# Optimization experiments

Hardware: AMD Instinct MI355X
Metric: run time of the kernel (lower is better)

Reference implementation:

```python
import jax, jax.numpy as jnp
import numpy as np

THRESHOLD = 0.3

def setup_inputs() -> dict:
    key = jax.random.key(0)
    ks = jax.random.split(key, 8)
    B, T, N, d = 4, 32, 1024, 2
    hd, od, hs, osz = 64, 64, 128, 2
    p = lambda k, sh: jax.random.normal(k, sh, jnp.float32) * 0.1
    return {
        "points": jax.random.uniform(ks[0], (B, T, N, d), jnp.float32),
        "W1": p(ks[1], (hd, d)),   "b1": jnp.zeros((hd,), jnp.float32),
        "W2": p(ks[2], (od, hd)),  "b2": jnp.zeros((od,), jnp.float32),
        "Wg": p(ks[3], (hd, od)),  "bg": jnp.zeros((hd,), jnp.float32),
        "Wih": p(ks[4], (3 * hs, hd)), "Whh": p(ks[5], (3 * hs, hs)),
        "bih": jnp.zeros((3 * hs,), jnp.float32), "bhh": jnp.zeros((3 * hs,), jnp.float32),
        "Wf": p(ks[6], (osz, hs)), "bf": jnp.zeros((osz,), jnp.float32),
    }

def _gcn_step(pts, W1, b1, W2, b2, Wg, bg):
    # pts: [N, d]. Torch detaches node features & adjacency (no grad to points).
    pts = jax.lax.stop_gradient(pts)
    dist = jnp.linalg.norm(pts[:, None, :] - pts[None, :, :], axis=2)  # [N,N]
    A = (dist < THRESHOLD).astype(pts.dtype)
    dinv = 1.0 / jnp.sqrt(A.sum(axis=1))          # rowsum >= 1 (self-loop)
    An = A * dinv[:, None] * dinv[None, :]        # D^{-1/2} A D^{-1/2}
    x = jax.nn.relu((An @ pts) @ W1.T + b1)       # [N, hd]
    x = jax.nn.relu((An @ x) @ W2.T + b2)         # [N, od]
    return x.mean(axis=0) @ Wg.T + bg             # [hd]

def reference(points, W1, b1, W2, b2, Wg, bg, Wih, Whh, bih, bhh, Wf, bf):
    # GCN per (batch, time): [B, T, hd]
    gcn = jax.vmap(jax.vmap(lambda p: _gcn_step(p, W1, b1, W2, b2, Wg, bg)))(points)
    H = Whh.shape[1]

    def gru_step(h, x):  # torch GRU gate order: r, z, n
        gi = x @ Wih.T + bih
        gh = h @ Whh.T + bhh
        ir, iz, inn = jnp.split(gi, 3)
        hr, hz, hn = jnp.split(gh, 3)
        r = jax.nn.sigmoid(ir + hr)
        z = jax.nn.sigmoid(iz + hz)
        n = jnp.tanh(inn + r * hn)
        h_new = (1.0 - z) * n + z * h
        return h_new, h_new

    h0 = jnp.zeros((H,), points.dtype)
    run = lambda xs: jax.lax.scan(gru_step, h0, xs)[1]   # [T, H]
    hs = jax.vmap(run)(gcn)                              # [B, T, H]
    y = hs @ Wf.T + bf                                   # [B, T, out]
    # torch: per-element gru_out.mean(dim=1, keepdim=True) on [1,T,out] -> [1,1,out], stacked -> [B,1,1,out]
    return y.mean(axis=1, keepdims=True)[:, :, None, :]
```

## Files before the change

kernel.cpp:

```cpp
#include <hip/hip_runtime.h>
#include <hip/hip_bf16.h>
#include <math.h>

#define N_PTS 1024
#define BT    128
typedef unsigned int u32;
typedef __attribute__((ext_vector_type(8))) short short8_t;
typedef __attribute__((ext_vector_type(4))) float f32x4;

__device__ __forceinline__ float bfi(u32 bits16) {
    union { u32 u; float f; } v; v.u = bits16 << 16; return v.f;
}
__device__ __forceinline__ unsigned short f2bf(float f) {
    union { float f; u32 u; } v; v.f = f;
    return (unsigned short)((v.u + 0x7FFFu + ((v.u >> 16) & 1u)) >> 16);
}
__device__ __forceinline__ u32 pkbf(float a, float b) {
    union { __hip_bfloat162 b2; u32 u; } cv;
    cv.b2 = __float22bfloat162_rn(make_float2(a, b));
    return cv.u;
}
__device__ __forceinline__ float ldf(const void* p, int i, bool bf) {
    return bf ? bfi(((const unsigned short*)p)[i]) : ((const float*)p)[i];
}
__device__ __forceinline__ float2 ldp(const void* pbase, int j, bool bf) {
    if (bf) {
        u32 w = ((const u32*)pbase)[j];
        return make_float2(bfi(w & 0xFFFFu), bfi(w >> 16));
    }
    return ((const float2*)pbase)[j];
}
__device__ __forceinline__ bool detect_bf16(const void* pts, int tid, int* s_flag) {
    if (tid < 64) {
        u32 w = ((const u32*)pts)[tid];
        float v = bfi(w & 0xFFFFu);
        bool ok = (v >= 0.0f) && (v <= 1.0f);
        unsigned long long m = __ballot(ok);
        if (tid == 0) *s_flag = (m == 0xFFFFFFFFFFFFFFFFull) ? 1 : 0;
    }
    __syncthreads();
    return *s_flag != 0;
}
__device__ __forceinline__ bool is_nb(float px, float py, float qx, float qy) {
    float dx = px - qx, dy = py - qy;
    float d2 = __fadd_rn(__fmul_rn(dx, dx), __fmul_rn(dy, dy));
    return d2 < 0.09f;
}
__device__ __forceinline__ const void* pts_base(const void* pts, int bt, bool bf) {
    return bf ? (const void*)((const unsigned short*)pts + (size_t)bt * N_PTS * 2)
              : (const void*)((const float*)pts + (size_t)bt * N_PTS * 2);
}
__device__ __forceinline__ void gload16(const u32* g, u32* l) {
    __builtin_amdgcn_global_load_lds((const __attribute__((address_space(1))) u32*)g,
                                     (__attribute__((address_space(3))) u32*)l, 16, 0, 0);
}
__device__ __forceinline__ float rdlane(float v, int i) {
    return __int_as_float(__builtin_amdgcn_readlane(__float_as_int(v), i));
}
__device__ __forceinline__ float sigm(float x) {
    return __fdividef(1.0f, 1.0f + __expf(-x));
}
__device__ __forceinline__ float tanh_f(float x) {
    return fmaf(2.0f, __fdividef(1.0f, 1.0f + __expf(-2.0f * x)), -1.0f);
}

__global__ __launch_bounds__(256) void k1_bm(const void* __restrict__ pts,
                                             float* __restrict__ dinv,
                                             float* __restrict__ gsum,
                                             u32* __restrict__ bm) {
    int blk = blockIdx.x, tid = threadIdx.x;
    int bt = blk >> 2, q = blk & 3;
    __shared__ float2 sp[N_PTS];
    __shared__ int s_flag;
    bool bf = detect_bf16(pts, tid, &s_flag);
    const void* pb = pts_base(pts, bt, bf);
    for (int j = tid; j < N_PTS; j += 256) sp[j] = ldp(pb, j, bf);
    if (blk < 32) gsum[blk * 256 + tid] = 0.0f;
    __syncthreads();
    int i = q * 256 + tid;
    float px = sp[i].x, py = sp[i].y;
    const float4* sp4 = (const float4*)sp;
    u32* bmrow = bm + (size_t)bt * 32768 + i;
    int cnt = 0;
    for (int c = 0; c < 32; c++) {
        u32 m = 0;
#pragma unroll
        for (int h = 0; h < 8; h++) {
            float4 s01 = sp4[c * 16 + 2 * h], s23 = sp4[c * 16 + 2 * h + 1];
            if (is_nb(px, py, s01.x, s01.y)) m |= 1u << (4 * h);
            if (is_nb(px, py, s01.z, s01.w)) m |= 1u << (4 * h + 1);
            if (is_nb(px, py, s23.x, s23.y)) m |= 1u << (4 * h + 2);
            if (is_nb(px, py, s23.z, s23.w)) m |= 1u << (4 * h + 3);
        }
        bmrow[c * 1024] = m;
        cnt += __popc(m);
    }
    dinv[bt * N_PTS + i] = 1.0f / sqrtf((float)cnt);
}

__global__ __launch_bounds__(256) void k3a_x1v(const void* __restrict__ pts,
                                               const void* __restrict__ W1,
                                               const void* __restrict__ b1,
                                               const float* __restrict__ dinv,
                                               const u32* __restrict__ bm,
                                               u32* __restrict__ x1vB) {
    __shared__ u32 pool[10944];
    __shared__ int s_flag;
    float* poolf = (float*)pool;
    float2* sud = (float2*)pool;
    u32* bmL = pool + 2048;
    float* sdiL = poolf + 10496;
    float* b1L = poolf + 10752;
    float* W1L = poolf + 10816;
    int tid = threadIdx.x, lane = tid & 63, w = tid >> 6;
    int l15 = lane & 15, quad = lane >> 4;
    int blk = blockIdx.x, bt = blk & 127, rowblk = blk >> 7;
    int rowbase = rowblk * 256;
    bool bf = detect_bf16(pts, tid, &s_flag);
    const void* pb = pts_base(pts, bt, bf);
    for (int j = tid; j < N_PTS; j += 256) {
        float2 p = ldp(pb, j, bf);
        float d = dinv[bt * N_PTS + j];
        sud[j] = make_float2(d * p.x, d * p.y);
    }
    sdiL[tid] = dinv[bt * N_PTS + rowbase + tid];
    for (int idx = tid; idx < 8192; idx += 256) {
        int c = idx >> 8, r = idx & 255;
        bmL[r * 33 + c] = bm[(size_t)bt * 32768 + c * 1024 + rowbase + r];
    }
    if (tid < 128) W1L[tid] = ldf(W1, tid, bf);
    if (tid < 64)  b1L[tid] = ldf(b1, tid, bf);
    __syncthreads();

    float w0v[4], w1v[4], b1v[4];
#pragma unroll
    for (int nb = 0; nb < 4; nb++) {
        int ch = nb * 16 + l15;
        w0v[nb] = W1L[2 * ch]; w1v[nb] = W1L[2 * ch + 1]; b1v[nb] = b1L[ch];
    }
    f32x4 acc[4][4];
#pragma unroll
    for (int rf = 0; rf < 4; rf++)
#pragma unroll
        for (int nb = 0; nb < 4; nb++)
#pragma unroll
            for (int r = 0; r < 4; r++) acc[rf][nb][r] = 0.0f;

    for (int ks = 0; ks < 32; ks++) {
        const float4* u4 = (const float4*)(sud + ks * 32 + quad * 8);
        float4 U0 = u4[0], U1 = u4[1], U2 = u4[2], U3 = u4[3];
        float pxd[8] = {U0.x, U0.z, U1.x, U1.z, U2.x, U2.z, U3.x, U3.z};
        float pyd[8] = {U0.y, U0.w, U1.y, U1.w, U2.y, U2.w, U3.y, U3.w};
        short8_t bz[4];
#pragma unroll
        for (int nb = 0; nb < 4; nb++) {
            union { short8_t v; u32 d[4]; } cv;
#pragma unroll
            for (int p = 0; p < 4; p++) {
                float z0 = fmaf(pxd[2 * p],     w0v[nb], pyd[2 * p]     * w1v[nb]);
                float z1 = fmaf(pxd[2 * p + 1], w0v[nb], pyd[2 * p + 1] * w1v[nb]);
                cv.d[p] = pkbf(z0, z1);
            }
            bz[nb] = cv.v;
        }
#pragma unroll
        for (int rf = 0; rf < 4; rf++) {
            u32 word = bmL[(w * 64 + rf * 16 + l15) * 33 + ks];
            u32 by = (word >> (quad * 8)) & 0xFFu;
            short8_t av;
#pragma unroll
            for (int i2 = 0; i2 < 8; i2++)
                av[i2] = (by & (1u << i2)) ? (short)0x3F80 : (short)0;
#pragma unroll
            for (int nb = 0; nb < 4; nb++)
                acc[rf][nb] = __builtin_amdgcn_mfma_f32_16x16x32_bf16(av, bz[nb], acc[rf][nb], 0, 0, 0);
        }
    }
    __syncthreads();
    u32* dumpX = pool + 2048;
#pragma unroll
    for (int rf = 0; rf < 4; rf++) {
        float4 dv = *(const float4*)(sdiL + w * 64 + rf * 16 + quad * 4);
        float dva[4] = {dv.x, dv.y, dv.z, dv.w};
#pragma unroll
        for (int nb = 0; nb < 4; nb++) {
            int ch = nb * 16 + l15;
            float xo[4];
#pragma unroll
            for (int r = 0; r < 4; r++) {
                float tq = fmaf(dva[r], acc[rf][nb][r], b1v[nb]);
                xo[r] = dva[r] * fmaxf(tq, 0.0f);
            }
            u32 dbase = (u32)(ch * 132 + w * 32 + rf * 8 + quad * 2);
            *(uint2*)(dumpX + dbase) = make_uint2(pkbf(xo[0], xo[1]), pkbf(xo[2], xo[3]));
        }
    }
    __syncthreads();
    int ch = tid >> 2, seg = tid & 3;
    u32* gbase = x1vB + ((size_t)(bt * 16 + rowblk * 4) * 64) * 36;
#pragma unroll
    for (int t4 = 0; t4 < 4; t4++) {
        const uint4* src = (const uint4*)(dumpX + ch * 132 + t4 * 32 + seg * 8);
        uint4 v0 = src[0], v1 = src[1];
        u32* dst = gbase + ((size_t)(t4 * 64 + ch)) * 36 + seg * 8;
        *(uint4*)dst = v0; *(uint4*)(dst + 4) = v1;
    }
}

__global__ __launch_bounds__(256) void k3_mfma(const void* __restrict__ pts,
                                               const void* __restrict__ W2,
                                               const void* __restrict__ b2,
                                               const float* __restrict__ dinv,
                                               const u32* __restrict__ bm,
                                               const u32* __restrict__ x1vB,
                                               float* __restrict__ gsum) {
    __shared__ u32 pool[15424];
    __shared__ int s_flag;
    float* poolf = (float*)pool;
    int tid = threadIdx.x, lane = tid & 63, w = tid >> 6;
    int l15 = lane & 15, quad = lane >> 4;
    int blk = blockIdx.x, bt = blk & 127, rowblk = blk >> 7;
    bool bf = detect_bf16(pts, tid, &s_flag);

    const u32* xg = x1vB + (size_t)bt * 36864;
    for (int it = w; it < 9; it += 4)
        gload16(xg + it * 256 + lane * 4, pool + 8192 + it * 256 + lane * 4);

    const u32* bg_ = bm + (size_t)bt * 32768 + rowblk * 256;
    for (int idx = tid; idx < 8192; idx += 256) {
        int c = idx >> 8, r = idx & 255;
        pool[idx] = bg_[c * 1024 + r];
    }
    unsigned short* W2B = (unsigned short*)(pool + 12800);
    for (int idx = tid; idx < 4096; idx += 256) {
        int o = idx >> 6, c = idx & 63;
        W2B[o * 72 + c] = f2bf(ldf(W2, idx, bf));
    }
    if (tid < 256) poolf[15104 + tid] = dinv[bt * N_PTS + rowblk * 256 + tid];
    if (tid < 64)  poolf[15360 + tid] = ldf(b2, tid, bf);

    f32x4 acc[4][4];
#pragma unroll
    for (int rf = 0; rf < 4; rf++)
#pragma unroll
        for (int nb = 0; nb < 4; nb++)
#pragma unroll
            for (int r = 0; r < 4; r++) acc[rf][nb][r] = 0.0f;

    for (int t = 0; t < 16; t++) {
        __syncthreads();
        if (t + 1 < 16) {
            u32* dst = pool + ((t & 1) ? 8192 : 10496);
            const u32* src = xg + (t + 1) * 2304;
            for (int it = w; it < 9; it += 4)
                gload16(src + it * 256 + lane * 4, dst + it * 256 + lane * 4);
        }
        const unsigned short* xf = (const unsigned short*)(pool + ((t & 1) ? 10496 : 8192));
#pragma unroll
        for (int ks = 0; ks < 2; ks++) {
            short8_t bq[4];
#pragma unroll
            for (int rf = 0; rf < 4; rf++) {
                u32 mw = pool[(2 * t + ks) * 256 + w * 64 + rf * 16 + l15];
                u32 by = (mw >> (quad * 8)) & 0xFFu;
                short8_t v;
#pragma unroll
                for (int i2 = 0; i2 < 8; i2++)
                    v[i2] = (by & (1u << i2)) ? (short)0x3F80 : (short)0;
                bq[rf] = v;
            }
#pragma unroll
            for (int nb = 0; nb < 4; nb++) {
                short8_t af = *(const short8_t*)(xf + (nb * 16 + l15) * 72 + ks * 32 + quad * 8);
#pragma unroll
                for (int rf = 0; rf < 4; rf++)
                    acc[rf][nb] = __builtin_amdgcn_mfma_f32_16x16x32_bf16(af, bq[rf], acc[rf][nb], 0, 0, 0);
            }
        }
    }
    __syncthreads();

    u32* dump = pool;
#pragma unroll
    for (int rf = 0; rf < 4; rf++) {
        int rn = w * 64 + rf * 16 + l15;
        float di = poolf[15104 + rn];
#pragma unroll
        for (int nb = 0; nb < 4; nb++) {
            u32 lo = (u32)f2bf(acc[rf][nb][0] * di) | ((u32)f2bf(acc[rf][nb][1] * di) << 16);
            u32 hi = (u32)f2bf(acc[rf][nb][2] * di) | ((u32)f2bf(acc[rf][nb][3] * di) << 16);
            u32* dst = dump + rn * 36 + nb * 8 + quad * 2;
            dst[0] = lo; dst[1] = hi;
        }
    }
    __syncthreads();
    f32x4 xacc[4][4];
#pragma unroll
    for (int ob = 0; ob < 4; ob++)
#pragma unroll
        for (int rf = 0; rf < 4; rf++)
#pragma unroll
            for (int r = 0; r < 4; r++) xacc[ob][rf][r] = 0.0f;
#pragma unroll
    for (int ks2 = 0; ks2 < 2; ks2++) {
        short8_t b2f[4];
#pragma unroll
        for (int rf = 0; rf < 4; rf++)
            b2f[rf] = *(const short8_t*)((const unsigned short*)dump +
                        (w * 64 + rf * 16 + l15) * 72 + ks2 * 32 + quad * 8);
#pragma unroll
        for (int ob = 0; ob < 4; ob++) {
            short8_t a2 = *(const short8_t*)(W2B + (ob * 16 + l15) * 72 + ks2 * 32 + quad * 8);
#pragma unroll
            for (int rf = 0; rf < 4; rf++)
                xacc[ob][rf] = __builtin_amdgcn_mfma_f32_16x16x32_bf16(a2, b2f[rf], xacc[ob][rf], 0, 0, 0);
        }
    }
#pragma unroll
    for (int ob = 0; ob < 4; ob++) {
#pragma unroll
        for (int r = 0; r < 4; r++) {
            int o = ob * 16 + quad * 4 + r;
            float bb = poolf[15360 + o];
            float s = 0.0f;
#pragma unroll
            for (int rf = 0; rf < 4; rf++) s += fmaxf(xacc[ob][rf][r] + bb, 0.0f);
            s += __shfl_down(s, 8, 16);
            s += __shfl_down(s, 4, 16);
            s += __shfl_down(s, 2, 16);
            s += __shfl_down(s, 1, 16);
            if (l15 == 0) atomicAdd(&gsum[bt * 64 + o], s);
        }
    }
}

__global__ __launch_bounds__(768, 1) void k4_all(const void* __restrict__ pts,
                                                 const void* __restrict__ Wg,
                                                 const void* __restrict__ bg,
                                                 const void* __restrict__ Wih,
                                                 const void* __restrict__ Whh,
                                                 const void* __restrict__ bih,
                                                 const void* __restrict__ bhh,
                                                 const void* __restrict__ Wf,
                                                 const void* __restrict__ bf_,
                                                 const float* __restrict__ gsum,
                                                 float* __restrict__ out) {
    int b = blockIdx.x, tid = threadIdx.x;
    __shared__ float s_gir[4096];
    __shared__ float s_giz[4096];
    __shared__ float s_gin[4096];
    __shared__ float sWgT[64 * 65];
    __shared__ float s_gm[2048];
    __shared__ float s_x[2048];
    __shared__ float s_pt[2 * 6 * 128];
    __shared__ int s_flag;
    bool bf = detect_bf16(pts, tid, &s_flag);
    for (int idx = tid; idx < 4096; idx += 768) {
        int o = idx >> 6, k = idx & 63;
        sWgT[k * 65 + o] = ldf(Wg, idx, bf);
    }
    for (int idx = tid; idx < 2048; idx += 768)
        s_gm[idx] = gsum[(size_t)b * 2048 + idx] * (1.0f / 1024.0f);
    __syncthreads();
    for (int idx = tid; idx < 2048; idx += 768) {
        int t = idx >> 6, c = idx & 63;
        float s0 = ldf(bg, c, bf), s1 = 0.f, s2 = 0.f, s3 = 0.f;
        const float* gm = s_gm + t * 64;
#pragma unroll
        for (int k = 0; k < 64; k += 4) {
            s0 = fmaf(sWgT[k * 65 + c],       gm[k],     s0);
            s1 = fmaf(sWgT[(k + 1) * 65 + c], gm[k + 1], s1);
            s2 = fmaf(sWgT[(k + 2) * 65 + c], gm[k + 2], s2);
            s3 = fmaf(sWgT[(k + 3) * 65 + c], gm[k + 3], s3);
        }
        s_x[idx] = (s0 + s1) + (s2 + s3);
    }
    __syncthreads();
    int hi = (tid >= 384) ? 1 : 0;
    int r = tid - hi * 384;
    int g = r >> 7;
    int cpart = r & 127;
    int lane = tid & 63;
    int wv = tid >> 6;
    float* gdst = (g == 0) ? s_gir : (g == 1) ? s_giz : s_gin;
    {
        float wvr[64];
        if (bf) {
#pragma unroll
            for (int k = 0; k < 64; k++) wvr[k] = bfi(((const unsigned short*)Wih)[r * 64 + k]);
        } else {
            const float4* wr = (const float4*)Wih + r * 16;
#pragma unroll
            for (int qq = 0; qq < 16; qq++) {
                float4 v = wr[qq];
                wvr[4*qq] = v.x; wvr[4*qq+1] = v.y; wvr[4*qq+2] = v.z; wvr[4*qq+3] = v.w;
            }
        }
        float br = ldf(bih, r, bf);
        for (int t = hi; t < 32; t += 2) {
            float xv = s_x[t * 64 + lane];
            float s0 = br, s1 = 0.f, s2 = 0.f, s3 = 0.f;
#pragma unroll
            for (int k = 0; k < 64; k += 4) {
                s0 = fmaf(wvr[k],     rdlane(xv, k),     s0);
                s1 = fmaf(wvr[k + 1], rdlane(xv, k + 1), s1);
                s2 = fmaf(wvr[k + 2], rdlane(xv, k + 2), s2);
                s3 = fmaf(wvr[k + 3], rdlane(xv, k + 3), s3);
            }
            gdst[t * 128 + cpart] = (s0 + s1) + (s2 + s3);
        }
    }
    float wh2[64];
    {
        int koff = hi * 64;
        if (bf) {
#pragma unroll
            for (int k = 0; k < 64; k++)
                wh2[k] = bfi(((const unsigned short*)Whh)[r * 128 + koff + k]);
        } else {
            const float4* wr = (const float4*)Whh + (r * 128 + koff) / 4;
#pragma unroll
            for (int qq = 0; qq < 16; qq++) {
                float4 v = wr[qq];
                wh2[4*qq] = v.x; wh2[4*qq+1] = v.y; wh2[4*qq+2] = v.z; wh2[4*qq+3] = v.w;
            }
        }
    }
    float bhr = hi ? 0.0f : ldf(bhh, r, bf);
    int slot = g * 2 + hi;
    int cg = hi * 64 + lane;
    float h_self = 0.0f, hsum = 0.0f;
    __syncthreads();

    for (int t = 0; t < 32; t++) {
        float s0 = bhr, s1 = 0.f, s2 = 0.f, s3 = 0.f;
#pragma unroll
        for (int k = 0; k < 64; k += 4) {
            s0 = fmaf(wh2[k],     rdlane(h_self, k),     s0);
            s1 = fmaf(wh2[k + 1], rdlane(h_self, k + 1), s1);
            s2 = fmaf(wh2[k + 2], rdlane(h_self, k + 2), s2);
            s3 = fmaf(wh2[k + 3], rdlane(h_self, k + 3), s3);
        }
        float* buf = s_pt + (t & 1) * 768;
        buf[slot * 128 + cpart] = (s0 + s1) + (s2 + s3);
        __syncthreads();
        float gr = s_gir[t * 128 + cg] + buf[0 * 128 + cg] + buf[1 * 128 + cg];
        float gz = s_giz[t * 128 + cg] + buf[2 * 128 + cg] + buf[3 * 128 + cg];
        float hn = buf[4 * 128 + cg] + buf[5 * 128 + cg];
        float rr = sigm(gr);
        float zz = sigm(gz);
        float gn = fmaf(rr, hn, s_gin[t * 128 + cg]);
        float n  = tanh_f(gn);
        float hnew = fmaf(zz, h_self - n, n);
        h_self = hnew; hsum += hnew;
    }
    float* sfin = s_gm;
    if (wv == 0) sfin[lane] = hsum;
    if (wv == 6) sfin[64 + lane] = hsum;
    __syncthreads();
    if (tid < 128) {
        float hm = sfin[tid] * (1.0f / 32.0f);
        sfin[256 + tid] = ldf(Wf, tid, bf) * hm;
        sfin[384 + tid] = ldf(Wf, 128 + tid, bf) * hm;
    }
    __syncthreads();
    if (tid < 2) {
        float s = ldf(bf_, tid, bf);
        for (int k = 0; k < 128; k++) s += sfin[256 + tid * 128 + k];
        out[b * 2 + tid] = s;
    }
}

extern "C" void kernel_launch(void* const* d_in, const int* in_sizes, int n_in,
                              void* d_out, int out_size, void* d_ws, size_t ws_size,
                              hipStream_t stream) {
    const void* pts = d_in[0];
    const void* W1  = d_in[1];
    const void* b1  = d_in[2];
    const void* W2  = d_in[3];
    const void* b2  = d_in[4];
    const void* Wg  = d_in[5];
    const void* bg  = d_in[6];
    const void* Wih = d_in[7];
    const void* Whh = d_in[8];
    const void* bih = d_in[9];
    const void* bhh = d_in[10];
    const void* Wf  = d_in[11];
    const void* bf_ = d_in[12];

    float* dinv = (float*)d_ws;
    float* gsum = dinv + (size_t)BT * N_PTS;
    u32*   bm   = (u32*)(gsum + BT * 64);
    u32*   x1vB = bm + (size_t)BT * 32768;

    k1_bm  <<<512, 256, 0, stream>>>(pts, dinv, gsum, bm);
    k3a_x1v<<<512, 256, 0, stream>>>(pts, W1, b1, dinv, bm, x1vB);
    k3_mfma<<<512, 256, 0, stream>>>(pts, W2, b2, dinv, bm, x1vB, gsum);
    k4_all <<<4, 768, 0, stream>>>(pts, Wg, bg, Wih, Whh, bih, bhh, Wf, bf_,
                                   gsum, (float*)d_out);
}
```

Measured before the change: 241.1 us.

## Use MFMA for GRU input projection and fp16 dot2 for recurrent matvec

Replaces the scalar readlane-based input-gate projection in the GRU kernel with bf16 MFMA tiles, using hi/lo bf16 splitting to keep accuracy close to fp32. The recurrent Whh matvec now keeps weights packed as fp16 pairs and uses fdot2 on a packed-half hidden state, which halves the readlanes per step. The gate update now runs only on the first 128 threads and publishes h through shared memory, adding a second barrier per timestep. This trades fp16 precision in the recurrence and an extra sync for fewer instructions per step; the GRU kernel is probably a small share of total time.

```diff
diff --git a/kernel.cpp b/kernel.cpp
--- a/kernel.cpp
+++ b/kernel.cpp
@@ -7,6 +7,17 @@
 typedef unsigned int u32;
 typedef __attribute__((ext_vector_type(8))) short short8_t;
 typedef __attribute__((ext_vector_type(4))) float f32x4;
+typedef __fp16 fp16x2 __attribute__((ext_vector_type(2)));
+typedef _Float16 f16x2 __attribute__((ext_vector_type(2)));
+
+#if defined(__has_builtin)
+#if __has_builtin(__builtin_amdgcn_fdot2)
+#define HAVE_FDOT2 1
+#endif
+#endif
+#ifndef HAVE_FDOT2
+#define HAVE_FDOT2 0
+#endif
 
 __device__ __forceinline__ float bfi(u32 bits16) {
     union { u32 u; float f; } v; v.u = bits16 << 16; return v.f;
@@ -20,6 +31,25 @@
     cv.b2 = __float22bfloat162_rn(make_float2(a, b));
     return cv.u;
 }
+__device__ __forceinline__ u32 pkh(float a, float b) {
+    union { fp16x2 h; u32 u; } c; c.h = __builtin_amdgcn_cvt_pkrtz(a, b); return c.u;
+}
+__device__ __forceinline__ unsigned short f16b(float v) {
+    union { fp16x2 h; unsigned short s[2]; } c;
+    c.h = __builtin_amdgcn_cvt_pkrtz(v, 0.0f);
+    return c.s[0];
+}
+#if HAVE_FDOT2
+__device__ __forceinline__ float fdot2h(u32 a, u32 b, float c) {
+    union { u32 u; f16x2 h; } A, B; A.u = a; B.u = b;
+    return __builtin_amdgcn_fdot2(A.h, B.h, c, false);
+}
+#else
+__device__ __forceinline__ float fdot2h(u32 a, u32 b, float c) {
+    union { u32 u; _Float16 h[2]; } A, B; A.u = a; B.u = b;
+    return fmaf((float)A.h[0], (float)B.h[0], fmaf((float)A.h[1], (float)B.h[1], c));
+}
+#endif
 __device__ __forceinline__ float ldf(const void* p, int i, bool bf) {
     return bf ? bfi(((const unsigned short*)p)[i]) : ((const float*)p)[i];
 }
@@ -54,8 +84,8 @@
     __builtin_amdgcn_global_load_lds((const __attribute__((address_space(1))) u32*)g,
                                      (__attribute__((address_space(3))) u32*)l, 16, 0, 0);
 }
-__device__ __forceinline__ float rdlane(float v, int i) {
-    return __int_as_float(__builtin_amdgcn_readlane(__float_as_int(v), i));
+__device__ __forceinline__ u32 rdlaneu(u32 v, int i) {
+    return (u32)__builtin_amdgcn_readlane((int)v, i);
 }
 __device__ __forceinline__ float sigm(float x) {
     return __fdividef(1.0f, 1.0f + __expf(-x));
@@ -352,9 +382,15 @@
     __shared__ float sWgT[64 * 65];
     __shared__ float s_gm[2048];
     __shared__ float s_x[2048];
-    __shared__ float s_pt[2 * 6 * 128];
+    __shared__ float s_pt[768];
+    __shared__ unsigned short s_hp[128];
     __shared__ int s_flag;
     bool bf = detect_bf16(pts, tid, &s_flag);
+    int lane = tid & 63, wv = tid >> 6;
+    int l15 = lane & 15, quad = lane >> 4;
+    int hi = (tid >= 384) ? 1 : 0;
+    int r = tid - hi * 384;
+
     for (int idx = tid; idx < 4096; idx += 768) {
         int o = idx >> 6, k = idx & 63;
         sWgT[k * 65 + o] = ldf(Wg, idx, bf);
@@ -375,98 +411,126 @@
         }
         s_x[idx] = (s0 + s1) + (s2 + s3);
     }
-    __syncthreads();
-    int hi = (tid >= 384) ? 1 : 0;
-    int r = tid - hi * 384;
-    int g = r >> 7;
+    u32 whp[32];
+    {
+        int koff = r * 128 + hi * 64;
+        if (bf) {
+            const u32* wp = (const u32*)Whh + koff / 2;
+#pragma unroll
+            for (int m = 0; m < 32; m++) {
+                u32 wq = wp[m];
+                whp[m] = pkh(bfi(wq & 0xFFFFu), bfi(wq >> 16));
+            }
+        } else {
+            const float2* wp = (const float2*)Whh + koff / 2;
+#pragma unroll
+            for (int m = 0; m < 32; m++) {
+                float2 v = wp[m];
+                whp[m] = pkh(v.x, v.y);
+            }
+        }
+    }
+    float bhr = hi ? 0.0f : ldf(bhh, r, bf);
+    __syncthreads();
+
+    {
+        short8_t Ah[2][2], Al[2][2];
+#pragma unroll
+        for (int mt = 0; mt < 2; mt++)
+#pragma unroll
+            for (int ks = 0; ks < 2; ks++) {
+                const float* xs = s_x + (mt * 16 + l15) * 64 + ks * 32 + quad * 8;
+                short8_t ah, al;
+#pragma unroll
+                for (int i = 0; i < 8; i++) {
+                    float v = xs[i];
+                    unsigned short hb = f2bf(v);
+                    ah[i] = (short)hb;
+                    al[i] = (short)f2bf(v - bfi(hb));
+                }
+                Ah[mt][ks] = ah; Al[mt][ks] = al;
+            }
+#pragma unroll
+        for (int ni = 0; ni < 2; ni++) {
+            int nt = wv * 2 + ni;
+            int c = nt * 16 + l15;
+            float bv = ldf(bih, c, bf);
+            short8_t Bh[2], Bl[2];
+#pragma unroll
+            for (int ks = 0; ks < 2; ks++) {
+                int base = c * 64 + ks * 32 + quad * 8;
+                short8_t bh, bl;
+#pragma unroll
+                for (int i = 0; i < 8; i++) {
+                    float v = ldf(Wih, base + i, bf);
+                    unsigned short hb = f2bf(v);
+                    bh[i] = (short)hb;
+                    bl[i] = (short)f2bf(v - bfi(hb));
+                }
+                Bh[ks] = bh; Bl[ks] = bl;
+            }
+            float* gdst = ((nt >> 3) == 0) ? s_gir : (((nt >> 3) == 1) ? s_giz : s_gin);
+            int cpart = (nt & 7) * 16 + l15;
+#pragma unroll
+            for (int mt = 0; mt < 2; mt++) {
+                f32x4 acc; acc[0] = bv; acc[1] = bv; acc[2] = bv; acc[3] = bv;
+#pragma unroll
+                for (int ks = 0; ks < 2; ks++) {
+                    acc = __builtin_amdgcn_mfma_f32_16x16x32_bf16(Ah[mt][ks], Bh[ks], acc, 0, 0, 0);
+                    acc = __builtin_amdgcn_mfma_f32_16x16x32_bf16(Ah[mt][ks], Bl[ks], acc, 0, 0, 0);
+                    acc = __builtin_amdgcn_mfma_f32_16x16x32_bf16(Al[mt][ks], Bh[ks], acc, 0, 0, 0);
+                }
+#pragma unroll
+                for (int rr2 = 0; rr2 < 4; rr2++) {
+                    int t = mt * 16 + quad * 4 + rr2;
+                    gdst[t * 128 + cpart] = acc[rr2];
+                }
+            }
+        }
+    }
+    int slot = (r >> 7) * 2 + hi;
     int cpart = r & 127;
-    int lane = tid & 63;
-    int wv = tid >> 6;
-    float* gdst = (g == 0) ? s_gir : (g == 1) ? s_giz : s_gin;
-    {
-        float wvr[64];
-        if (bf) {
-#pragma unroll
-            for (int k = 0; k < 64; k++) wvr[k] = bfi(((const unsigned short*)Wih)[r * 64 + k]);
-        } else {
-            const float4* wr = (const float4*)Wih + r * 16;
-#pragma unroll
-            for (int qq = 0; qq < 16; qq++) {
-                float4 v = wr[qq];
-                wvr[4*qq] = v.x; wvr[4*qq+1] = v.y; wvr[4*qq+2] = v.z; wvr[4*qq+3] = v.w;
-            }
-        }
-        float br = ldf(bih, r, bf);
-        for (int t = hi; t < 32; t += 2) {
-            float xv = s_x[t * 64 + lane];
-            float s0 = br, s1 = 0.f, s2 = 0.f, s3 = 0.f;
-#pragma unroll
-            for (int k = 0; k < 64; k += 4) {
-                s0 = fmaf(wvr[k],     rdlane(xv, k),     s0);
-                s1 = fmaf(wvr[k + 1], rdlane(xv, k + 1), s1);
-                s2 = fmaf(wvr[k + 2], rdlane(xv, k + 2), s2);
-                s3 = fmaf(wvr[k + 3], rdlane(xv, k + 3), s3);
-            }
-            gdst[t * 128 + cpart] = (s0 + s1) + (s2 + s3);
-        }
-    }
-    float wh2[64];
-    {
-        int koff = hi * 64;
-        if (bf) {
-#pragma unroll
-            for (int k = 0; k < 64; k++)
-                wh2[k] = bfi(((const unsigned short*)Whh)[r * 128 + koff + k]);
-        } else {
-            const float4* wr = (const float4*)Whh + (r * 128 + koff) / 4;
-#pragma unroll
-            for (int qq = 0; qq < 16; qq++) {
-                float4 v = wr[qq];
-                wh2[4*qq] = v.x; wh2[4*qq+1] = v.y; wh2[4*qq+2] = v.z; wh2[4*qq+3] = v.w;
-            }
-        }
-    }
-    float bhr = hi ? 0.0f : ldf(bhh, r, bf);
-    int slot = g * 2 + hi;
-    int cg = hi * 64 + lane;
     float h_self = 0.0f, hsum = 0.0f;
+    u32 hpreg = 0;
     __syncthreads();
 
     for (int t = 0; t < 32; t++) {
         float s0 = bhr, s1 = 0.f, s2 = 0.f, s3 = 0.f;
 #pragma unroll
-        for (int k = 0; k < 64; k += 4) {
-            s0 = fmaf(wh2[k],     rdlane(h_self, k),     s0);
-            s1 = fmaf(wh2[k + 1], rdlane(h_self, k + 1), s1);
-            s2 = fmaf(wh2[k + 2], rdlane(h_self, k + 2), s2);
-            s3 = fmaf(wh2[k + 3], rdlane(h_self, k + 3), s3);
-        }
-        float* buf = s_pt + (t & 1) * 768;
-        buf[slot * 128 + cpart] = (s0 + s1) + (s2 + s3);
+        for (int m = 0; m < 32; m += 4) {
+            s0 = fdot2h(whp[m],     rdlaneu(hpreg, m),     s0);
+            s1 = fdot2h(whp[m + 1], rdlaneu(hpreg, m + 1), s1);
+            s2 = fdot2h(whp[m + 2], rdlaneu(hpreg, m + 2), s2);
+            s3 = fdot2h(whp[m + 3], rdlaneu(hpreg, m + 3), s3);
+        }
+        s_pt[slot * 128 + cpart] = (s0 + s1) + (s2 + s3);
         __syncthreads();
-        float gr = s_gir[t * 128 + cg] + buf[0 * 128 + cg] + buf[1 * 128 + cg];
-        float gz = s_giz[t * 128 + cg] + buf[2 * 128 + cg] + buf[3 * 128 + cg];
-        float hn = buf[4 * 128 + cg] + buf[5 * 128 + cg];
-        float rr = sigm(gr);
-        float zz = sigm(gz);
-        float gn = fmaf(rr, hn, s_gin[t * 128 + cg]);
-        float n  = tanh_f(gn);
-        float hnew = fmaf(zz, h_self - n, n);
-        h_self = hnew; hsum += hnew;
-    }
-    float* sfin = s_gm;
-    if (wv == 0) sfin[lane] = hsum;
-    if (wv == 6) sfin[64 + lane] = hsum;
+        if (tid < 128) {
+            int c = tid;
+            float gr = s_gir[t * 128 + c] + s_pt[c]       + s_pt[128 + c];
+            float gz = s_giz[t * 128 + c] + s_pt[256 + c] + s_pt[384 + c];
+            float hn = s_pt[512 + c] + s_pt[640 + c];
+            float rr = sigm(gr);
+            float zz = sigm(gz);
+            float n  = tanh_f(fmaf(rr, hn, s_gin[t * 128 + c]));
+            float hnew = fmaf(zz, h_self - n, n);
+            h_self = hnew; hsum += hnew;
+            s_hp[c] = f16b(hnew);
+        }
+        __syncthreads();
+        hpreg = ((const u32*)s_hp)[hi * 32 + (lane & 31)];
+    }
+    if (tid < 128) s_gm[tid] = hsum;
     __syncthreads();
     if (tid < 128) {
-        float hm = sfin[tid] * (1.0f / 32.0f);
-        sfin[256 + tid] = ldf(Wf, tid, bf) * hm;
-        sfin[384 + tid] = ldf(Wf, 128 + tid, bf) * hm;
+        float hm = s_gm[tid] * (1.0f / 32.0f);
+        s_gm[256 + tid] = ldf(Wf, tid, bf) * hm;
+        s_gm[384 + tid] = ldf(Wf, 128 + tid, bf) * hm;
     }
     __syncthreads();
     if (tid < 2) {
         float s = ldf(bf_, tid, bf);
-        for (int k = 0; k < 128; k++) s += sfin[256 + tid * 128 + k];
+        for (int k = 0; k < 128; k++) s += s_gm[256 + tid * 128 + k];
         out[b * 2 + tid] = s;
     }
 }
```

Result: no change. 240.8 us (-0.1%).
